# Kernel optimization log

Measured on AMD Instinct MI355X. Metric: run time of the kernel, lower is better.

Reference implementation:

```python
import jax, jax.numpy as jnp
import numpy as np

NUM_HEADS = 8

def setup_inputs() -> dict:
    key = jax.random.key(0)
    ks = jax.random.split(key, 12)
    B, C, H, W = 4, 256, 64, 64
    QK = 256
    NSP = 256
    x = jax.random.normal(ks[0], (B, C, H, W), dtype=jnp.float32)
    affinity_matrix = jax.random.uniform(ks[1], (B, NSP, H * W), dtype=jnp.float32)
    norm_w = 1.0 + 0.02 * jax.random.normal(ks[2], (C,), dtype=jnp.float32)
    norm_b = 0.02 * jax.random.normal(ks[3], (C,), dtype=jnp.float32)
    Wq = 0.02 * jax.random.normal(ks[4], (QK, C), dtype=jnp.float32)
    Wk = 0.02 * jax.random.normal(ks[5], (QK, C), dtype=jnp.float32)
    Wv = 0.02 * jax.random.normal(ks[6], (C, C), dtype=jnp.float32)
    Wsp = 0.02 * jax.random.normal(ks[7], (QK, C), dtype=jnp.float32)
    lepe_w = 0.02 * jax.random.normal(ks[8], (C, 1, 3, 3), dtype=jnp.float32)  # depthwise OIHW
    lepe_b = 0.02 * jax.random.normal(ks[9], (C,), dtype=jnp.float32)
    return {"x": x, "affinity_matrix": affinity_matrix, "norm_w": norm_w,
            "norm_b": norm_b, "Wq": Wq, "Wk": Wk, "Wv": Wv, "Wsp": Wsp,
            "lepe_w": lepe_w, "lepe_b": lepe_b, "num_spixels": NSP}


def _layernorm2d(x, w, b, eps=1e-6):
    # LayerNorm over channel dim of NCHW input
    xp = x.transpose(0, 2, 3, 1)  # B,H,W,C
    mu = xp.mean(-1, keepdims=True)
    var = ((xp - mu) ** 2).mean(-1, keepdims=True)
    xn = (xp - mu) * jax.lax.rsqrt(var + eps) * w + b
    return xn.transpose(0, 3, 1, 2)


def _sgca(x, affinity_matrix, norm_w, norm_b, Wq, Wk, Wv, Wsp, lepe_w, lepe_b, num_spixels):
    B, C, H, W = x.shape
    HW = H * W
    h = NUM_HEADS
    qk_dim = Wq.shape[0]
    dqk = qk_dim // h
    dv = C // h
    scale = (C // h) ** -0.5

    xn = _layernorm2d(x, norm_w, norm_b)

    # superpixel aggregation: b (hw) c
    x_flat = xn.reshape(B, C, HW).transpose(0, 2, 1)  # B,HW,C
    stoken = jnp.einsum('bmn,bnc->bmc', affinity_matrix, x_flat)
    stoken = stoken / (affinity_matrix.sum(-1, keepdims=True) + 1e-16)  # B,nsp,C

    # sp projection -> B,h,dqk,nsp
    st = jnp.einsum('bmc,qc->bmq', stoken, Wsp).transpose(0, 2, 1)
    st = st.reshape(B, h, dqk, num_spixels)

    # 1x1 conv projections
    q = jnp.einsum('oc,bchw->bohw', Wq, xn).reshape(B, h, dqk, HW)
    k = jnp.einsum('oc,bchw->bohw', Wk, xn).reshape(B, h, dqk, HW)
    vx = jnp.einsum('oc,bchw->bohw', Wv, xn)  # B,C,H,W
    v = vx.reshape(B, h, dv, HW)

    # LePE: depthwise 3x3 conv on v(x)
    lepe = jax.lax.conv_general_dilated(
        vx, lepe_w, window_strides=(1, 1), padding=((1, 1), (1, 1)),
        feature_group_count=C, dimension_numbers=('NCHW', 'OIHW', 'NCHW'))
    lepe = lepe + lepe_b[None, :, None, None]
    # faithful to original: [B,C,HW] -> permute -> [B,HW,C] -> reshape B,C,H,W
    lepe = lepe.reshape(B, C, HW).transpose(0, 2, 1).reshape(B, C, H, W)

    # stage 1: k^T @ stoken, softmax over HW axis
    s_attn = jnp.einsum('bhdn,bhdm->bhnm', k, st) * scale  # B,h,HW,nsp
    s_attn = jax.nn.softmax(s_attn, axis=-2)
    s_out = jnp.einsum('bhdn,bhnm->bhdm', v, s_attn)  # B,h,dv,nsp

    # stage 2: stoken^T @ q, softmax over nsp axis
    x_attn = jnp.einsum('bhdm,bhdn->bhmn', st, q) * scale  # B,h,nsp,HW
    x_attn = jax.nn.softmax(x_attn, axis=-2)
    x_out = jnp.einsum('bhdm,bhmn->bhdn', s_out, x_attn).reshape(B, C, H, W)

    return x_out + lepe


def reference(x, affinity_matrix, norm_w, norm_b, Wq, Wk, Wv, Wsp, lepe_w, lepe_b, num_spixels):
    return _sgca(x, affinity_matrix, norm_w, norm_b, Wq, Wk, Wv, Wsp, lepe_w, lepe_b, num_spixels)
```

## Files before the change

kernel.cpp:

```cpp
#include <hip/hip_runtime.h>
#include <hip/hip_bf16.h>

#define BATCH 4
#define CCH   256
#define HWHW  4096
#define NSP   256
#define NHEAD 8
#define SCALE 0.17677669529663689f
#define PLANE 1048576L

typedef short bf16x8 __attribute__((ext_vector_type(8)));
typedef short bf16x4 __attribute__((ext_vector_type(4)));
typedef float f32x4  __attribute__((ext_vector_type(4)));

__device__ __forceinline__ short f2bs(float f) {
    __hip_bfloat16 h = __float2bfloat16(f);
    return *(short*)&h;
}
__device__ __forceinline__ bf16x8 cvt8(float4 a, float4 b) {
    bf16x8 p;
    p[0] = f2bs(a.x); p[1] = f2bs(a.y); p[2] = f2bs(a.z); p[3] = f2bs(a.w);
    p[4] = f2bs(b.x); p[5] = f2bs(b.y); p[6] = f2bs(b.z); p[7] = f2bs(b.w);
    return p;
}
__device__ __forceinline__ void gll16(const __hip_bfloat16* g, __hip_bfloat16* l) {
    __builtin_amdgcn_global_load_lds(
        (const __attribute__((address_space(1))) unsigned int*)(const void*)g,
        (__attribute__((address_space(3))) unsigned int*)(void*)l,
        16, 0, 0);
}

__global__ __launch_bounds__(512)
void ln_fused_kernel(const float* __restrict__ x, const float* __restrict__ w,
                     const float* __restrict__ bb,
                     const float* __restrict__ Wq, const float* __restrict__ Wk,
                     const float* __restrict__ Wv, const float* __restrict__ Wsp,
                     __hip_bfloat16* __restrict__ xn_cn,
                     __hip_bfloat16* __restrict__ xn_nc,
                     __hip_bfloat16* __restrict__ wbf)
{
    __shared__ float ps[32][64], pss[32][64];
    __shared__ float mus[64], rstds[64];
    __shared__ float wls[256], bls[256];
    int blk = blockIdx.x;
    int t = threadIdx.x;
    if (blk >= 256) {
        int sel = blk - 256;
        const float* src = (sel == 0) ? Wq : (sel == 1) ? Wk : (sel == 2) ? Wv : Wsp;
        __hip_bfloat16* dst = wbf + sel * 65536;
        for (int i = t * 4; i < 65536; i += 2048) {
            float4 f = *(const float4*)(src + i);
            __hip_bfloat16 p[4];
            p[0] = __float2bfloat16(f.x); p[1] = __float2bfloat16(f.y);
            p[2] = __float2bfloat16(f.z); p[3] = __float2bfloat16(f.w);
            *(int2*)(dst + i) = *(int2*)p;
        }
        return;
    }
    int b = blk >> 6;
    int n0 = (blk & 63) * 64;
    int pg = t & 15;
    int cq = t >> 4;
    if (t < 256) { wls[t] = w[t]; bls[t] = bb[t]; }

    const float* xp = x + ((long)(b * CCH + cq * 8)) * HWHW + n0 + pg * 4;
    float4 v[8];
#pragma unroll
    for (int i = 0; i < 8; ++i) v[i] = *(const float4*)(xp + (long)i * HWHW);
    float4 s = {0.f,0.f,0.f,0.f}, ss = {0.f,0.f,0.f,0.f};
#pragma unroll
    for (int i = 0; i < 8; ++i) {
        s.x += v[i].x; s.y += v[i].y; s.z += v[i].z; s.w += v[i].w;
        ss.x += v[i].x * v[i].x; ss.y += v[i].y * v[i].y;
        ss.z += v[i].z * v[i].z; ss.w += v[i].w * v[i].w;
    }
    *(float4*)&ps[cq][pg * 4]  = s;
    *(float4*)&pss[cq][pg * 4] = ss;
    __syncthreads();
    if (t < 64) {
        float S = 0.f, SS = 0.f;
#pragma unroll
        for (int q = 0; q < 32; ++q) { S += ps[q][t]; SS += pss[q][t]; }
        float mu = S * (1.f / 256.f);
        float var = SS * (1.f / 256.f) - mu * mu;
        mus[t] = mu; rstds[t] = rsqrtf(var + 1e-6f);
    }
    __syncthreads();
    float4 mu4 = *(float4*)&mus[pg * 4];
    float4 rs4 = *(float4*)&rstds[pg * 4];

    bf16x8 pk[4];
#pragma unroll
    for (int i = 0; i < 8; ++i) {
        int c = cq * 8 + i;
        float wc = wls[c], bc = bls[c];
        short h0 = f2bs((v[i].x - mu4.x) * rs4.x * wc + bc);
        short h1 = f2bs((v[i].y - mu4.y) * rs4.y * wc + bc);
        short h2 = f2bs((v[i].z - mu4.z) * rs4.z * wc + bc);
        short h3 = f2bs((v[i].w - mu4.w) * rs4.w * wc + bc);
        pk[0][i] = h0; pk[1][i] = h1; pk[2][i] = h2; pk[3][i] = h3;
        bf16x4 q; q[0] = h0; q[1] = h1; q[2] = h2; q[3] = h3;
        *(bf16x4*)(xn_cn + ((long)(b * CCH + c)) * HWHW + n0 + pg * 4) = q;
    }
#pragma unroll
    for (int j = 0; j < 4; ++j)
        *(bf16x8*)(xn_nc + ((long)b * HWHW + n0 + pg * 4 + j) * CCH + cq * 8) = pk[j];
}

template <int OUTK, int ASTAGE, bool ROWSUM, int NTL>
__device__ __forceinline__ void gemm_body(
    const void* __restrict__ Av, const __hip_bfloat16* __restrict__ B,
    void* __restrict__ Cptr, int bx, int by, int bz,
    int N, int K, int kChunk, int kShift,
    long aStrideZ, long bStrideZ, long cStrideZ,
    float* __restrict__ rsPart,
    __hip_bfloat16* __restrict__ Asm, __hip_bfloat16* __restrict__ Bsm,
    float* __restrict__ rsl)
{
    int z = bz;
    int b = z >> kShift;
    int ch = z & ((1 << kShift) - 1);
    int t = threadIdx.x;
    int lane = t & 63, w = t >> 6;
    int l15 = lane & 15, quad = lane >> 4;
    int Mt = by * 64, Nt = bx * 64 * NTL;

    if (ASTAGE == 2 && t < 64) {
        float s = 0.f;
#pragma unroll
        for (int pl = 0; pl < 8; ++pl) s += rsPart[((b * 8 + pl) << 8) + Mt + t];
        rsl[t] = s;
    }

    long aOff = (long)b * aStrideZ + (long)ch * kChunk
        + (long)(Mt + w * 16 + l15) * K + quad * 8;
    const __hip_bfloat16* aSrcH = (const __hip_bfloat16*)Av + aOff;
    const float*          aSrcF = (const float*)Av + aOff;
    const __hip_bfloat16* bSrc = B + (long)b * bStrideZ + (long)ch * kChunk
        + (long)(Nt + w * 16 + l15) * K + quad * 8;

    f32x4 acc[NTL][2][2];
#pragma unroll
    for (int nt = 0; nt < NTL; ++nt)
#pragma unroll
        for (int i = 0; i < 2; ++i)
#pragma unroll
            for (int j = 0; j < 2; ++j) acc[nt][i][j] = f32x4{0.f,0.f,0.f,0.f};
    f32x4 rs0 = {0.f,0.f,0.f,0.f}, rs1 = rs0;
    bf16x8 onesf;
    { short o = (l15 == 0) ? (short)0x3F80 : (short)0;
      onesf = bf16x8{o, o, o, o, o, o, o, o}; }
    int wm = (w & 1) * 2, wn = (w >> 1) * 2;

    float4 pf0, pf1, pf2, pf3;
    if (ASTAGE == 1) {
        pf0 = *(const float4*)(aSrcF);      pf1 = *(const float4*)(aSrcF + 4);
        pf2 = *(const float4*)(aSrcF + 32); pf3 = *(const float4*)(aSrcF + 36);
    }

    const bf16x8* AsmU = (const bf16x8*)Asm;
    const bf16x8* BsmU = (const bf16x8*)Bsm;

    for (int k0 = 0; k0 < kChunk; k0 += 64) {
        if (ASTAGE == 0) {
            gll16(aSrcH + k0,      Asm + w * 512);
            gll16(aSrcH + k0 + 32, Asm + 2048 + w * 512);
        } else if (ASTAGE == 1) {
            *(bf16x8*)&Asm[t * 8]        = cvt8(pf0, pf1);
            *(bf16x8*)&Asm[2048 + t * 8] = cvt8(pf2, pf3);
        } else {
#pragma unroll
            for (int kh = 0; kh < 2; ++kh) {
                float4 s0 = {0.f,0.f,0.f,0.f}, s1 = {0.f,0.f,0.f,0.f};
#pragma unroll
                for (int pl = 0; pl < 8; ++pl) {
                    const float* p = aSrcF + (long)pl * 65536 + k0 + kh * 32;
                    float4 u0 = *(const float4*)p, u1 = *(const float4*)(p + 4);
                    s0.x += u0.x; s0.y += u0.y; s0.z += u0.z; s0.w += u0.w;
                    s1.x += u1.x; s1.y += u1.y; s1.z += u1.z; s1.w += u1.w;
                }
                *(bf16x8*)&Asm[kh * 2048 + t * 8] = cvt8(s0, s1);
            }
        }
#pragma unroll
        for (int nt = 0; nt < NTL; ++nt) {
            gll16(bSrc + (long)nt * 64 * K + k0,      Bsm + nt * 4096 + w * 512);
            gll16(bSrc + (long)nt * 64 * K + k0 + 32, Bsm + nt * 4096 + 2048 + w * 512);
        }
        __syncthreads();
        if (ASTAGE == 1 && k0 + 64 < kChunk) {
            const float* nx = aSrcF + k0 + 64;
            pf0 = *(const float4*)nx;        pf1 = *(const float4*)(nx + 4);
            pf2 = *(const float4*)(nx + 32); pf3 = *(const float4*)(nx + 36);
        }
#pragma unroll
        for (int kh = 0; kh < 2; ++kh) {
            bf16x8 a0 = AsmU[kh * 256 + wm * 64 + lane];
            bf16x8 a1 = AsmU[kh * 256 + (wm + 1) * 64 + lane];
            if (ROWSUM) {
                rs0 = __builtin_amdgcn_mfma_f32_16x16x32_bf16(a0, onesf, rs0, 0, 0, 0);
                rs1 = __builtin_amdgcn_mfma_f32_16x16x32_bf16(a1, onesf, rs1, 0, 0, 0);
            }
#pragma unroll
            for (int nt = 0; nt < NTL; ++nt) {
                bf16x8 b0 = BsmU[nt * 512 + kh * 256 + wn * 64 + lane];
                bf16x8 b1 = BsmU[nt * 512 + kh * 256 + (wn + 1) * 64 + lane];
                acc[nt][0][0] = __builtin_amdgcn_mfma_f32_16x16x32_bf16(a0, b0, acc[nt][0][0], 0, 0, 0);
                acc[nt][0][1] = __builtin_amdgcn_mfma_f32_16x16x32_bf16(a0, b1, acc[nt][0][1], 0, 0, 0);
                acc[nt][1][0] = __builtin_amdgcn_mfma_f32_16x16x32_bf16(a1, b0, acc[nt][1][0], 0, 0, 0);
                acc[nt][1][1] = __builtin_amdgcn_mfma_f32_16x16x32_bf16(a1, b1, acc[nt][1][1], 0, 0, 0);
            }
        }
        __syncthreads();
    }
    if (ROWSUM && bx == 0 && (w >> 1) == 0 && l15 == 0) {
#pragma unroll
        for (int r = 0; r < 4; ++r) {
            rsPart[(long)z * 256 + Mt + wm * 16 + quad * 4 + r]       = rs0[r];
            rsPart[(long)z * 256 + Mt + (wm + 1) * 16 + quad * 4 + r] = rs1[r];
        }
    }
#pragma unroll
    for (int nt = 0; nt < NTL; ++nt)
#pragma unroll
        for (int i = 0; i < 2; ++i)
#pragma unroll
            for (int j = 0; j < 2; ++j)
#pragma unroll
                for (int r = 0; r < 4; ++r) {
                    int m = Mt + (wm + i) * 16 + quad * 4 + r;
                    int n = Nt + nt * 64 + (wn + j) * 16 + l15;
                    float val = acc[nt][i][j][r];
                    if (ASTAGE == 2) val /= (rsl[m - Mt] + 1e-16f);
                    long off = (long)z * cStrideZ + (long)m * N + n;
                    if (OUTK == 0) ((float*)Cptr)[off] = val;
                    else ((__hip_bfloat16*)Cptr)[off] = __float2bfloat16(val);
                }
}

__global__ __launch_bounds__(256)
void mega1_kernel(const float* __restrict__ aff,
                  const __hip_bfloat16* __restrict__ xn_cn,
                  const __hip_bfloat16* __restrict__ xn_nc,
                  const __hip_bfloat16* __restrict__ wbf,
                  __hip_bfloat16* __restrict__ qk_nc,
                  __hip_bfloat16* __restrict__ v_cn,
                  float* __restrict__ stoken_part,
                  float* __restrict__ rs_part)
{
    __shared__ __hip_bfloat16 Asm[4096];
    __shared__ __hip_bfloat16 Bsm[4 * 4096];
    int blk = blockIdx.x;
    if (blk < 128) {
        int i = blk;
        gemm_body<0, 1, true, 4>(aff, xn_cn, stoken_part,
            0, i & 3, i >> 2, 256, 4096, 512, 3,
            PLANE, PLANE, 65536L, rs_part, Asm, Bsm, nullptr);
    } else if (blk < 2176) {
        int i = blk - 128;
        gemm_body<1, 0, false, 1>(xn_nc, wbf, qk_nc,
            i & 7, (i >> 3) & 63, i >> 9, 512, 256, 256, 0,
            PLANE, 0L, 2 * PLANE, nullptr, Asm, Bsm, nullptr);
    } else {
        int i = blk - 2176;
        gemm_body<1, 0, false, 1>(wbf + 2 * 65536, xn_nc, v_cn,
            i & 63, (i >> 6) & 3, i >> 8, 4096, 256, 256, 0,
            0L, PLANE, PLANE, nullptr, Asm, Bsm, nullptr);
    }
}

__global__ __launch_bounds__(256)
void stmd_kernel(const float* __restrict__ part,
                 const __hip_bfloat16* __restrict__ wsp,
                 __hip_bfloat16* __restrict__ st_md,
                 float* __restrict__ rs_part)
{
    __shared__ __hip_bfloat16 Asm[4096];
    __shared__ __hip_bfloat16 Bsm[4096];
    __shared__ float rsl[64];
    int i = blockIdx.x;
    gemm_body<1, 2, false, 1>(part, wsp, st_md,
        i & 3, (i >> 2) & 3, i >> 4, 256, 256, 256, 0,
        524288L, 0L, 65536L, rs_part, Asm, Bsm, rsl);
}

__device__ __forceinline__
void stage1_dev(char* smem, int chunk, int bh,
                const __hip_bfloat16* __restrict__ qk_nc,
                const __hip_bfloat16* __restrict__ v_cn,
                const __hip_bfloat16* __restrict__ st_md,
                __hip_bfloat16* __restrict__ opart)
{
    __hip_bfloat16* Es  = (__hip_bfloat16*)smem;
    __hip_bfloat16* sts = (__hip_bfloat16*)(smem + 36864);
    const int b = bh >> 3, h = bh & 7;
    const int t = threadIdx.x, lane = t & 63, w = t >> 6;
    const int l15 = lane & 15, quad = lane >> 4;
    const int n0 = chunk * 256;

    {
        const int4* src = (const int4*)(st_md + ((long)(b * 256 + t)) * 256 + h * 32);
        int4* dst = (int4*)&sts[t * 40];
        dst[0] = src[0]; dst[1] = src[1]; dst[2] = src[2]; dst[3] = src[3];
    }
    __syncthreads();
    bf16x8 afrag[16];
#pragma unroll
    for (int mt = 0; mt < 16; ++mt)
        afrag[mt] = *(const bf16x8*)&sts[(mt * 16 + l15) * 40 + quad * 8];
    bf16x8 onesf;
    { short o = (l15 == 0) ? (short)0x3F80 : (short)0;
      onesf = bf16x8{o, o, o, o, o, o, o, o}; }

    f32x4 occ[4][3];
#pragma unroll
    for (int i = 0; i < 4; ++i)
#pragma unroll
        for (int j = 0; j < 3; ++j) occ[i][j] = f32x4{0.f,0.f,0.f,0.f};

    for (int sub = 0; sub < 4; ++sub) {
        const int nbase = n0 + sub * 64;
        bf16x8 kf = *(const bf16x8*)(qk_nc + ((long)b * 4096 + nbase + 16 * w + l15) * 512 + 256 + h * 32 + quad * 8);
#pragma unroll
        for (int mt = 0; mt < 16; ++mt) {
            f32x4 s = __builtin_amdgcn_mfma_f32_16x16x32_bf16(afrag[mt], kf, f32x4{0.f,0.f,0.f,0.f}, 0, 0, 0);
#pragma unroll
            for (int r = 0; r < 4; ++r)
                Es[(mt * 16 + quad * 4 + r) * 72 + 16 * w + l15] =
                    __float2bfloat16(__expf(s[r] * SCALE));
        }
        __syncthreads();
#pragma unroll
        for (int ks = 0; ks < 2; ++ks) {
            bf16x8 bf0 = *(const bf16x8*)(v_cn + ((long)(b * 256 + h * 32 + l15)) * 4096 + nbase + ks * 32 + quad * 8);
            bf16x8 bf1 = *(const bf16x8*)(v_cn + ((long)(b * 256 + h * 32 + 16 + l15)) * 4096 + nbase + ks * 32 + quad * 8);
#pragma unroll
            for (int mi = 0; mi < 4; ++mi) {
                bf16x8 af = *(const bf16x8*)&Es[(64 * w + mi * 16 + l15) * 72 + ks * 32 + quad * 8];
                occ[mi][0] = __builtin_amdgcn_mfma_f32_16x16x32_bf16(af, bf0, occ[mi][0], 0, 0, 0);
                occ[mi][1] = __builtin_amdgcn_mfma_f32_16x16x32_bf16(af, bf1, occ[mi][1], 0, 0, 0);
                occ[mi][2] = __builtin_amdgcn_mfma_f32_16x16x32_bf16(af, onesf, occ[mi][2], 0, 0, 0);
            }
        }
        __syncthreads();
    }
    __hip_bfloat16* tb = Es;
#pragma unroll
    for (int mi = 0; mi < 4; ++mi)
#pragma unroll
        for (int jt = 0; jt < 3; ++jt) {
            if (jt == 2 && l15 != 0) continue;
            int col = jt * 16 + l15;
#pragma unroll
            for (int r = 0; r < 4; ++r) {
                int m = 64 * w + mi * 16 + quad * 4 + r;
                tb[col * 264 + m] = __float2bfloat16(occ[mi][jt][r]);
            }
        }
    __syncthreads();
    int* og = (int*)(opart) + (long)(chunk * 32 + bh) * 4224;
    const int* tbi = (const int*)tb;
#pragma unroll
    for (int i = 0; i < 17; ++i) {
        int idx = t + i * 256;
        if (idx < 4224) {
            int row = idx >> 7, off = idx & 127;
            og[idx] = tbi[row * 132 + off];
        }
    }
}

__device__ __forceinline__
void lepe_dev(char* smem, int bx, int cy, int b,
              const __hip_bfloat16* __restrict__ v_cn,
              const float* __restrict__ lw, const float* __restrict__ lb,
              __hip_bfloat16* __restrict__ lepe_cn)
{
    __hip_bfloat16* in_t    = (__hip_bfloat16*)smem;
    __hip_bfloat16* tile_bf = (__hip_bfloat16*)(smem + 24576);
    float* wls = (float*)(smem + 41472);
    float* bls = (float*)(smem + 42624);
    const int c0 = cy * 32;
    const int t = threadIdx.x;
    const int n0 = bx * 256, r0 = bx * 4;

    for (int i = t; i < 288; i += 256) wls[i] = lw[c0 * 9 + i];
    if (t < 32)  bls[t] = lb[c0 + t];
#pragma unroll
    for (int i = 0; i < 6; ++i) {
        int vi = t + i * 256;
        int ch = vi / 48;
        int off = (vi % 48) * 8;
        int g = (r0 - 1) * 64 + off;
        int4 val = {0, 0, 0, 0};
        if ((unsigned)g < 4096u)
            val = *(const int4*)(v_cn + (((long)(b * CCH + c0 + ch)) << 12) + g);
        *(int4*)&in_t[ch * 384 + off] = val;
    }
    __syncthreads();

    const int lane = t & 63, w = t >> 6;
#pragma unroll
    for (int i = 0; i < 8; ++i) {
        int ch = w * 8 + i;
        float cr[6], lf[6], rf[6];
#pragma unroll
        for (int rr = 0; rr < 6; ++rr) {
            cr[rr] = (float)in_t[ch * 384 + rr * 64 + lane];
            float lv = __shfl_up(cr[rr], 1);
            float rv = __shfl_down(cr[rr], 1);
            lf[rr] = (lane == 0) ? 0.f : lv;
            rf[rr] = (lane == 63) ? 0.f : rv;
        }
        float w0 = wls[ch*9+0], w1 = wls[ch*9+1], w2 = wls[ch*9+2];
        float w3 = wls[ch*9+3], w4 = wls[ch*9+4], w5 = wls[ch*9+5];
        float w6 = wls[ch*9+6], w7 = wls[ch*9+7], w8 = wls[ch*9+8];
        float bias = bls[ch];
#pragma unroll
        for (int r = 0; r < 4; ++r) {
            float acc = bias
                + lf[r]   * w0 + cr[r]   * w1 + rf[r]   * w2
                + lf[r+1] * w3 + cr[r+1] * w4 + rf[r+1] * w5
                + lf[r+2] * w6 + cr[r+2] * w7 + rf[r+2] * w8;
            tile_bf[(r * 64 + lane) * 33 + ch] = __float2bfloat16(acc);
        }
    }
    __syncthreads();
#pragma unroll
    for (int i = 0; i < 32; ++i) {
        int idx = t + i * 256;
        int nl = idx >> 5, cj = idx & 31;
        int sp = n0 + nl;
        lepe_cn[((long)(b * CCH + (sp >> 4)) << 12) + (nl & 15) * 256 + c0 + cj] =
            tile_bf[nl * 33 + cj];
    }
}

__global__ __launch_bounds__(256)
void mega2_kernel(const __hip_bfloat16* __restrict__ qk_nc,
                  const __hip_bfloat16* __restrict__ v_cn,
                  const __hip_bfloat16* __restrict__ st_md,
                  __hip_bfloat16* __restrict__ opart,
                  const float* __restrict__ lw, const float* __restrict__ lb,
                  __hip_bfloat16* __restrict__ lepe_cn)
{
    __shared__ __align__(16) char smem[57344];
    int blk = blockIdx.x;
    if (blk < 512) {
        stage1_dev(smem, blk & 15, blk >> 4, qk_nc, v_cn, st_md, opart);
    } else {
        int j = blk - 512;
        lepe_dev(smem, j & 15, (j >> 4) & 7, j >> 7, v_cn, lw, lb, lepe_cn);
    }
}

__global__ __launch_bounds__(256)
void merge1_kernel(const __hip_bfloat16* __restrict__ opart, __hip_bfloat16* __restrict__ sout)
{
    int t = blockIdx.x * 256 + threadIdx.x;
    int m = t & 255;
    int d = (t >> 8) & 31;
    int bh = t >> 13;
    float num = 0.f, den = 0.f;
    for (int ch = 0; ch < 16; ++ch) {
        long base = (long)((ch * 32 + bh) * 33) * 256 + m;
        num += (float)opart[base + (long)d * 256];
        den += (float)opart[base + 32 * 256];
    }
    sout[(long)bh * 8192 + d * 256 + m] = __float2bfloat16(num / den);
}

__global__ __launch_bounds__(256)
void stage2_mfma(const __hip_bfloat16* __restrict__ qk_nc,
                 const __hip_bfloat16* __restrict__ st_md,
                 const __hip_bfloat16* __restrict__ sout_bf,
                 const __hip_bfloat16* __restrict__ lepe_cn,
                 float* __restrict__ out)
{
    __shared__ __hip_bfloat16 Es2[64 * 264];
    __shared__ __hip_bfloat16 sts[256 * 40];
    __shared__ __hip_bfloat16 sos[32 * 264];
    __shared__ float o_t[32 * 68];
    const int chunk = blockIdx.x, bh = blockIdx.y;
    const int b = bh >> 3, h = bh & 7;
    const int t = threadIdx.x, lane = t & 63, w = t >> 6;
    const int l15 = lane & 15, quad = lane >> 4;
    const int n0 = chunk * 256;

    {
        const int4* src = (const int4*)(st_md + ((long)(b * 256 + t)) * 256 + h * 32);
        int4* dst = (int4*)&sts[t * 40];
        dst[0] = src[0]; dst[1] = src[1]; dst[2] = src[2]; dst[3] = src[3];
    }
    {
        int row = t >> 3, seg = t & 7;
        const int4* src = (const int4*)(sout_bf + (long)bh * 8192 + row * 256 + seg * 32);
        int4* dst = (int4*)&sos[row * 264 + seg * 32];
        dst[0] = src[0]; dst[1] = src[1]; dst[2] = src[2]; dst[3] = src[3];
    }
    __syncthreads();
    bf16x8 stfrag[4];
#pragma unroll
    for (int mt = 0; mt < 4; ++mt)
        stfrag[mt] = *(const bf16x8*)&sts[(64 * w + mt * 16 + l15) * 40 + quad * 8];
    bf16x8 onesf;
    { short o = (l15 == 0) ? (short)0x3F80 : (short)0;
      onesf = bf16x8{o, o, o, o, o, o, o, o}; }

    for (int sub = 0; sub < 4; ++sub) {
        const int nbase = n0 + sub * 64;
#pragma unroll
        for (int nt = 0; nt < 4; ++nt) {
            bf16x8 qf = *(const bf16x8*)(qk_nc + ((long)b * 4096 + nbase + nt * 16 + l15) * 512 + h * 32 + quad * 8);
#pragma unroll
            for (int mt = 0; mt < 4; ++mt) {
                f32x4 s = __builtin_amdgcn_mfma_f32_16x16x32_bf16(qf, stfrag[mt], f32x4{0.f,0.f,0.f,0.f}, 0, 0, 0);
#pragma unroll
                for (int r = 0; r < 4; ++r)
                    Es2[(nt * 16 + quad * 4 + r) * 264 + 64 * w + mt * 16 + l15] =
                        __float2bfloat16(__expf(s[r] * SCALE));
            }
        }
        __syncthreads();
        f32x4 o0 = {0.f,0.f,0.f,0.f}, o1 = o0, o2 = o0;
#pragma unroll
        for (int ks = 0; ks < 8; ++ks) {
            bf16x8 af = *(const bf16x8*)&Es2[(16 * w + l15) * 264 + ks * 32 + quad * 8];
            bf16x8 b0 = *(const bf16x8*)&sos[(l15) * 264 + ks * 32 + quad * 8];
            bf16x8 b1 = *(const bf16x8*)&sos[(16 + l15) * 264 + ks * 32 + quad * 8];
            o0 = __builtin_amdgcn_mfma_f32_16x16x32_bf16(af, b0, o0, 0, 0, 0);
            o1 = __builtin_amdgcn_mfma_f32_16x16x32_bf16(af, b1, o1, 0, 0, 0);
            o2 = __builtin_amdgcn_mfma_f32_16x16x32_bf16(af, onesf, o2, 0, 0, 0);
        }
        __syncthreads();
#pragma unroll
        for (int r = 0; r < 4; ++r) {
            float den = __shfl(o2[r], lane & 48);
            float inv = 1.f / den;
            o_t[(l15) * 68 + 16 * w + quad * 4 + r]      = o0[r] * inv;
            o_t[(16 + l15) * 68 + 16 * w + quad * 4 + r] = o1[r] * inv;
        }
        __syncthreads();
        {
            int row = t >> 3, coff = (t & 7) * 8;
            long gb = ((long)(b * 256 + h * 32 + row)) * 4096 + nbase + coff;
            int4 lp4 = *(const int4*)(lepe_cn + gb);
            const __hip_bfloat16* lp = (const __hip_bfloat16*)&lp4;
            const float* sp = &o_t[row * 68 + coff];
            float4 r0, r1;
            r0.x = sp[0] + (float)lp[0]; r0.y = sp[1] + (float)lp[1];
            r0.z = sp[2] + (float)lp[2]; r0.w = sp[3] + (float)lp[3];
            r1.x = sp[4] + (float)lp[4]; r1.y = sp[5] + (float)lp[5];
            r1.z = sp[6] + (float)lp[6]; r1.w = sp[7] + (float)lp[7];
            *(float4*)(out + gb)     = r0;
            *(float4*)(out + gb + 4) = r1;
        }
        __syncthreads();
    }
}

extern "C" void kernel_launch(void* const* d_in, const int* in_sizes, int n_in,
                              void* d_out, int out_size, void* d_ws, size_t ws_size,
                              hipStream_t stream)
{
    const float* x    = (const float*)d_in[0];
    const float* aff  = (const float*)d_in[1];
    const float* nw   = (const float*)d_in[2];
    const float* nb   = (const float*)d_in[3];
    const float* Wq   = (const float*)d_in[4];
    const float* Wk   = (const float*)d_in[5];
    const float* Wv   = (const float*)d_in[6];
    const float* Wsp  = (const float*)d_in[7];
    const float* lw   = (const float*)d_in[8];
    const float* lb   = (const float*)d_in[9];
    float* out = (float*)d_out;

    float* ws = (float*)d_ws;
    const long P = PLANE;
    __hip_bfloat16* qk_nc  = (__hip_bfloat16*)(ws);
    __hip_bfloat16* v_cn   = (__hip_bfloat16*)(ws + 4 * P);
    __hip_bfloat16* xn_cn  = (__hip_bfloat16*)(ws + 6 * P);
    __hip_bfloat16* xn_nc  = (__hip_bfloat16*)(ws + 8 * P);
    __hip_bfloat16* lepe_cn= (__hip_bfloat16*)(ws + 10 * P);
    float* stoken_part = ws + 14 * P;
    __hip_bfloat16* opart = (__hip_bfloat16*)(ws + 16 * P);
    float* tail        = ws + 16 * P + 2162688;
    __hip_bfloat16* wbf       = (__hip_bfloat16*)tail;
    __hip_bfloat16* st_md     = (__hip_bfloat16*)(tail + 262144);
    __hip_bfloat16* sout_bf   = (__hip_bfloat16*)(tail + 393216);
    float* rs_part = tail + 525312;

    ln_fused_kernel<<<260, 512, 0, stream>>>(x, nw, nb, Wq, Wk, Wv, Wsp,
                                             xn_cn, xn_nc, wbf);
    mega1_kernel<<<3200, 256, 0, stream>>>(aff, xn_cn, xn_nc, wbf,
                                           qk_nc, v_cn, stoken_part, rs_part);
    stmd_kernel<<<64, 256, 0, stream>>>(stoken_part, wbf + 3 * 65536, st_md, rs_part);
    mega2_kernel<<<1024, 256, 0, stream>>>(qk_nc, v_cn, st_md, opart, lw, lb, lepe_cn);
    merge1_kernel<<<1024, 256, 0, stream>>>(opart, sout_bf);
    stage2_mfma<<<dim3(16, 32), 256, 0, stream>>>(qk_nc, st_md, sout_bf, lepe_cn, out);
}
```

Before: 208.0 us.

## Add one-shot K=256 GEMM path for QK/V projections in mega1 kernel

```diff
diff --git a/kernel.cpp b/kernel.cpp
--- a/kernel.cpp
+++ b/kernel.cpp
@@ -107,6 +107,53 @@
         *(bf16x8*)(xn_nc + ((long)b * HWHW + n0 + pg * 4 + j) * CCH + cq * 8) = pk[j];
 }
 
+__device__ __forceinline__ void gemm_k256_oneshot(
+    const __hip_bfloat16* __restrict__ A, const __hip_bfloat16* __restrict__ B,
+    __hip_bfloat16* __restrict__ C, int bx, int by, int bz,
+    int N, long aStrideZ, long bStrideZ, long cStrideZ,
+    __hip_bfloat16* __restrict__ Asm)
+{
+    const int K = 256;
+    const int t = threadIdx.x, lane = t & 63, w = t >> 6;
+    const int l15 = lane & 15, quad = lane >> 4;
+    const int Mt = by * 64, Nt = bx * 64;
+    const __hip_bfloat16* aSrc = A + (long)bz * aStrideZ
+        + (long)(Mt + w * 16 + l15) * K + quad * 8;
+#pragma unroll
+    for (int p = 0; p < 8; ++p)
+        gll16(aSrc + p * 32, Asm + ((w * 8 + p) << 9));
+
+    const int wm = (w & 1) * 2, wn = (w >> 1) * 2;
+    const __hip_bfloat16* b0p = B + (long)bz * bStrideZ
+        + (long)(Nt + wn * 16 + l15) * K + quad * 8;
+    const __hip_bfloat16* b1p = b0p + 16 * K;
+    f32x4 acc00 = {0.f,0.f,0.f,0.f}, acc01 = acc00, acc10 = acc00, acc11 = acc00;
+    __syncthreads();
+#pragma unroll
+    for (int s = 0; s < 8; ++s) {
+        bf16x8 a0 = *(const bf16x8*)&Asm[((wm * 8 + s) << 9) + lane * 8];
+        bf16x8 a1 = *(const bf16x8*)&Asm[(((wm + 1) * 8 + s) << 9) + lane * 8];
+        bf16x8 b0 = *(const bf16x8*)(b0p + s * 32);
+        bf16x8 b1 = *(const bf16x8*)(b1p + s * 32);
+        acc00 = __builtin_amdgcn_mfma_f32_16x16x32_bf16(a0, b0, acc00, 0, 0, 0);
+        acc01 = __builtin_amdgcn_mfma_f32_16x16x32_bf16(a0, b1, acc01, 0, 0, 0);
+        acc10 = __builtin_amdgcn_mfma_f32_16x16x32_bf16(a1, b0, acc10, 0, 0, 0);
+        acc11 = __builtin_amdgcn_mfma_f32_16x16x32_bf16(a1, b1, acc11, 0, 0, 0);
+    }
+    f32x4 accs[2][2] = {{acc00, acc01}, {acc10, acc11}};
+#pragma unroll
+    for (int i = 0; i < 2; ++i)
+#pragma unroll
+        for (int j = 0; j < 2; ++j)
+#pragma unroll
+            for (int r = 0; r < 4; ++r) {
+                int m = Mt + (wm + i) * 16 + quad * 4 + r;
+                int n = Nt + (wn + j) * 16 + l15;
+                C[(long)bz * cStrideZ + (long)m * N + n] =
+                    __float2bfloat16(accs[i][j][r]);
+            }
+}
+
 template <int OUTK, int ASTAGE, bool ROWSUM, int NTL>
 __device__ __forceinline__ void gemm_body(
     const void* __restrict__ Av, const __hip_bfloat16* __restrict__ B,
@@ -134,8 +181,7 @@
 
     long aOff = (long)b * aStrideZ + (long)ch * kChunk
         + (long)(Mt + w * 16 + l15) * K + quad * 8;
-    const __hip_bfloat16* aSrcH = (const __hip_bfloat16*)Av + aOff;
-    const float*          aSrcF = (const float*)Av + aOff;
+    const float* aSrcF = (const float*)Av + aOff;
     const __hip_bfloat16* bSrc = B + (long)b * bStrideZ + (long)ch * kChunk
         + (long)(Nt + w * 16 + l15) * K + quad * 8;
 
@@ -162,10 +208,7 @@
     const bf16x8* BsmU = (const bf16x8*)Bsm;
 
     for (int k0 = 0; k0 < kChunk; k0 += 64) {
-        if (ASTAGE == 0) {
-            gll16(aSrcH + k0,      Asm + w * 512);
-            gll16(aSrcH + k0 + 32, Asm + 2048 + w * 512);
-        } else if (ASTAGE == 1) {
+        if (ASTAGE == 1) {
             *(bf16x8*)&Asm[t * 8]        = cvt8(pf0, pf1);
             *(bf16x8*)&Asm[2048 + t * 8] = cvt8(pf2, pf3);
         } else {
@@ -238,7 +281,7 @@
                 }
 }
 
-__global__ __launch_bounds__(256)
+__global__ __launch_bounds__(256, 4)
 void mega1_kernel(const float* __restrict__ aff,
                   const __hip_bfloat16* __restrict__ xn_cn,
                   const __hip_bfloat16* __restrict__ xn_nc,
@@ -248,8 +291,10 @@
                   float* __restrict__ stoken_part,
                   float* __restrict__ rs_part)
 {
-    __shared__ __hip_bfloat16 Asm[4096];
-    __shared__ __hip_bfloat16 Bsm[4 * 4096];
+    __shared__ __align__(16) char smem[40960];
+    __hip_bfloat16* Asm = (__hip_bfloat16*)smem;
+    __hip_bfloat16* Bsm = (__hip_bfloat16*)(smem + 8192);
+    __hip_bfloat16* Aos = (__hip_bfloat16*)smem;
     int blk = blockIdx.x;
     if (blk < 128) {
         int i = blk;
@@ -258,14 +303,12 @@
             PLANE, PLANE, 65536L, rs_part, Asm, Bsm, nullptr);
     } else if (blk < 2176) {
         int i = blk - 128;
-        gemm_body<1, 0, false, 1>(xn_nc, wbf, qk_nc,
-            i & 7, (i >> 3) & 63, i >> 9, 512, 256, 256, 0,
-            PLANE, 0L, 2 * PLANE, nullptr, Asm, Bsm, nullptr);
+        gemm_k256_oneshot(xn_nc, wbf, qk_nc,
+            i & 7, (i >> 3) & 63, i >> 9, 512, PLANE, 0L, 2 * PLANE, Aos);
     } else {
         int i = blk - 2176;
-        gemm_body<1, 0, false, 1>(wbf + 2 * 65536, xn_nc, v_cn,
-            i & 63, (i >> 6) & 3, i >> 8, 4096, 256, 256, 0,
-            0L, PLANE, PLANE, nullptr, Asm, Bsm, nullptr);
+        gemm_k256_oneshot(wbf + 2 * 65536, xn_nc, v_cn,
+            i & 63, (i >> 6) & 3, i >> 8, 4096, 0L, PLANE, PLANE, Aos);
     }
 }
 
```

Result: slower. 216.2 us (+3.9%).
